# Optimization experiments

Hardware: AMD Instinct MI355X
Metric: run time of the kernel (lower is better)

## Reference

```python
import jax, jax.numpy as jnp
import numpy as np

K = 9                # snake kernel size
CENTER = K // 2
EXT = 1.0            # extend_scope
EPS = 1e-5           # GroupNorm eps (torch default)


def conv2d(x, w, b, stride, padding):
    out = jax.lax.conv_general_dilated(
        x, w, window_strides=stride, padding=padding,
        dimension_numbers=("NCHW", "OIHW", "NCHW"))
    return out + b[None, :, None, None]


def group_norm(x, gamma, beta, groups):
    B, C, H, W = x.shape
    xg = x.reshape(B, groups, C // groups, H, W)
    mu = xg.mean(axis=(2, 3, 4), keepdims=True)
    var = xg.var(axis=(2, 3, 4), keepdims=True)
    xn = ((xg - mu) / jnp.sqrt(var + EPS)).reshape(B, C, H, W)
    return xn * gamma[None, :, None, None] + beta[None, :, None, None]


def setup_inputs() -> dict:
    key = jax.random.key(0)
    ks = jax.random.split(key, 6)
    B, Cin, Cout, H, W = 4, 64, 64, 128, 128
    x = jax.random.normal(ks[0], (B, Cin, H, W), jnp.float32)
    w_off = jax.random.normal(ks[1], (2 * K, Cin, 3, 3), jnp.float32) * 0.05
    b_off = jax.random.normal(ks[2], (2 * K,), jnp.float32) * 0.01
    g_gn_off = jnp.ones((2 * K,), jnp.float32)
    b_gn_off = jnp.zeros((2 * K,), jnp.float32)
    w_dsc = jax.random.normal(ks[3], (Cout, Cin, K, 1), jnp.float32) * 0.05
    b_dsc = jax.random.normal(ks[4], (Cout,), jnp.float32) * 0.01
    g_gn = jnp.ones((Cout,), jnp.float32)
    b_gn = jnp.zeros((Cout,), jnp.float32)
    return {"x": x, "w_off": w_off, "b_off": b_off,
            "g_gn_off": g_gn_off, "b_gn_off": b_gn_off,
            "w_dsc": w_dsc, "b_dsc": b_dsc, "g_gn": g_gn, "b_gn": b_gn}


def reference(x, w_off, b_off, g_gn_off, b_gn_off, w_dsc, b_dsc, g_gn, b_gn):
    B, Cin, H, W = x.shape
    # offset branch: conv3x3 -> GN(K groups over 2K chans) -> tanh
    off = conv2d(x, w_off, b_off, (1, 1), "SAME")
    off = jnp.tanh(group_norm(off, g_gn_off, b_gn_off, K))
    y_off = off[:, :K]                              # morph=0 uses y offsets, [B,K,H,W]

    # cumulative offsets outward from the kernel center (center entry = 0)
    upper = jnp.cumsum(y_off[:, CENTER + 1:], axis=1)
    lower = jnp.flip(jnp.cumsum(jnp.flip(y_off[:, :CENTER], axis=1), axis=1), axis=1)
    y_off_new = jnp.concatenate(
        [lower, jnp.zeros_like(y_off[:, :1]), upper], axis=1)   # [B,K,H,W]

    # coordinate maps (pixel space)
    y_coord = jnp.arange(H, dtype=x.dtype)[None, None, :, None] + EXT * y_off_new
    x_spread = jnp.linspace(-CENTER, CENTER, K).astype(x.dtype)
    x_coord = jnp.broadcast_to(
        jnp.arange(W, dtype=x.dtype)[None, None, None, :]
        + x_spread[None, :, None, None], y_coord.shape)
    # rearrange b k h w -> b (h k) w
    y_map = y_coord.transpose(0, 2, 1, 3).reshape(B, H * K, W)
    x_map = x_coord.transpose(0, 2, 1, 3).reshape(B, H * K, W)

    # bilinear grid_sample, align_corners=True; clamp-to-range == torch's
    # _coordinate_map_scaling(clamp + [-1,1] normalize) then grid_sample
    yc = jnp.clip(y_map, 0.0, H - 1.0)
    xc = jnp.clip(x_map, 0.0, W - 1.0)
    y0 = jnp.floor(yc); x0 = jnp.floor(xc)
    wy = yc - y0; wx = xc - x0
    y0i = y0.astype(jnp.int32); x0i = x0.astype(jnp.int32)
    y1i = jnp.minimum(y0i + 1, H - 1); x1i = jnp.minimum(x0i + 1, W - 1)

    def samp(f, y0i, y1i, x0i, x1i, wy, wx):
        # f: [C,H,W]; indices/weights: [K*H, W] -> [C, K*H, W]
        v00 = f[:, y0i, x0i]; v01 = f[:, y0i, x1i]
        v10 = f[:, y1i, x0i]; v11 = f[:, y1i, x1i]
        return (v00 * (1 - wy) * (1 - wx) + v01 * (1 - wy) * wx
                + v10 * wy * (1 - wx) + v11 * wy * wx)

    deformed = jax.vmap(samp)(x, y0i, y1i, x0i, x1i, wy, wx)  # [B,C,K*H,W]

    # snake conv: kernel (K,1), stride (K,1), then GN(out//4) + ReLU
    out = conv2d(deformed, w_dsc, b_dsc, (K, 1), "VALID")      # [B,Cout,H,W]
    out = group_norm(out, g_gn, b_gn, w_dsc.shape[0] // 4)
    return jax.nn.relu(out)
```

## Files before the change

kernel.cpp:

```cpp
#include <hip/hip_runtime.h>
#include <hip/hip_bf16.h>
#include <math.h>

#define B 4
#define C 64
#define H 128
#define W 128
#define KK 9
#define CENTER 4
#define HW (H*W)
#define HP 130
#define WP 130

typedef __attribute__((ext_vector_type(8))) short short8;
typedef __attribute__((ext_vector_type(4))) float f4;

#define OFF_OFFT   0
#define OFF_XB     786432
#define OFF_WB     2949632
#define OFF_WOB    2968064
#define OFF_CSUM   2972672
#define OFF_OSUM   2980864

__device__ __forceinline__ unsigned bf16pack(float a, float b) {
    unsigned ua = __builtin_bit_cast(unsigned, a) + 0x8000u;
    unsigned ub = __builtin_bit_cast(unsigned, b) + 0x8000u;
    return __builtin_amdgcn_perm(ub, ua, 0x07060302);
}

__device__ __forceinline__ unsigned lerp_pack(unsigned a, unsigned b, float fw) {
    float alo = __builtin_bit_cast(float, a << 16);
    float ahi = __builtin_bit_cast(float, a & 0xffff0000u);
    float blo = __builtin_bit_cast(float, b << 16);
    float bhi = __builtin_bit_cast(float, b & 0xffff0000u);
    float slo = alo + fw * (blo - alo);
    float shi = ahi + fw * (bhi - ahi);
    return bf16pack(slo, shi);
}

__device__ __forceinline__ float fast_tanh(float x) {
    float e = __expf(2.f * x);
    return 1.f - 2.f * __builtin_amdgcn_rcpf(e + 1.f);
}

__global__ __launch_bounds__(256) void k_prep(const float* __restrict__ x,
                                              const float* __restrict__ w_dsc,
                                              const float* __restrict__ w_off,
                                              unsigned short* __restrict__ xb,
                                              unsigned short* __restrict__ wb,
                                              unsigned short* __restrict__ wob,
                                              float* __restrict__ csum) {
    int bid = blockIdx.x;
    int tid = threadIdx.x;
    if (bid < 2048) {
        __shared__ float lt[64 * 33];
        int xcd = bid & 7, i = bid >> 3;
        int c = i & 3, hc = (i >> 2) & 15, b = i >> 6;
        int h = (xcd << 4) | hc;
        int w0 = c * 32;
        int ciA = tid >> 2, gA = tid & 3;
        int wlB = tid >> 3, cgB = tid & 7;

        if (c == 0 && tid < 8)
            *(uint4*)(xb + ((size_t)(b * HP + h + 1) * WP) * 64 + tid * 8)
                = make_uint4(0, 0, 0, 0);
        if (c == 3 && tid < 8)
            *(uint4*)(xb + (((size_t)(b * HP + h + 1) * WP) + WP - 1) * 64 + tid * 8)
                = make_uint4(0, 0, 0, 0);
        {
            const float* src = x + ((size_t)(b * C + ciA) * HW) + h * W + w0 + gA * 8;
            float4 v0 = *(const float4*)src;
            float4 v1 = *(const float4*)(src + 4);
            float* d = lt + ciA * 33 + gA * 8;
            d[0] = v0.x; d[1] = v0.y; d[2] = v0.z; d[3] = v0.w;
            d[4] = v1.x; d[5] = v1.y; d[6] = v1.z; d[7] = v1.w;
        }
        __syncthreads();
        {
            unsigned u[4];
#pragma unroll
            for (int i2 = 0; i2 < 4; i2++) {
                float lo = lt[(cgB * 8 + 2 * i2)     * 33 + wlB];
                float hi = lt[(cgB * 8 + 2 * i2 + 1) * 33 + wlB];
                u[i2] = bf16pack(lo, hi);
            }
            *(uint4*)(xb + ((size_t)((b * HP + h + 1) * WP + w0 + wlB + 1)) * 64 + cgB * 8) =
                make_uint4(u[0], u[1], u[2], u[3]);
        }
    } else if (bid < 2048 + 8) {
        int r = bid - 2048;
        int b = r >> 1, which = r & 1;
        unsigned short* dst = xb + ((size_t)(b * HP + which * (HP - 1)) * WP) * 64;
        for (int t = tid; t < WP * 64 / 8; t += 256)
            *(uint4*)(dst + t * 8) = make_uint4(0, 0, 0, 0);
    } else if (bid < 2048 + 8 + 180) {
        int idx = (bid - (2048 + 8)) * 256 + tid;
        if (idx < KK * C * C) {
            int k  = idx >> 12;
            int r  = idx & 4095;
            int co = r >> 6;
            int ci = r & 63;
            unsigned u = __builtin_bit_cast(unsigned, w_dsc[(co * C + ci) * KK + k]);
            u = (u + 0x7fffu + ((u >> 16) & 1u)) >> 16;
            wb[idx] = (unsigned short)u;
        } else if (idx < KK * C * C + 9 * 16 * 64) {
            int r   = idx - KK * C * C;
            int tap = r >> 10;
            int j   = (r >> 6) & 15;
            int ci  = r & 63;
            float v = (j < 10) ? w_off[(j * C + ci) * 9 + tap] : 0.f;
            unsigned u = __builtin_bit_cast(unsigned, v);
            u = (u + 0x7fffu + ((u >> 16) & 1u)) >> 16;
            wob[r] = (unsigned short)u;
        }
    } else {
        int z = bid - (2048 + 8 + 180);
        int base = z * 1024 + tid * 4;
        *(f4*)(csum + base) = 0;
    }
}

__global__ __launch_bounds__(256, 4) void k_offconv(const unsigned short* __restrict__ xb,
                                                    const unsigned short* __restrict__ wob,
                                                    const float* __restrict__ b_off,
                                                    float* __restrict__ offT,
                                                    float* __restrict__ osum16) {
    __shared__ unsigned short wlds[1152 * 8];
    __shared__ float red[80];
    int bid = blockIdx.x;
    int xcd  = bid & 7;
    int i    = bid >> 3;
    int b    = i >> 5;
    int rest = i & 31;
    int h    = (xcd << 4) | (rest >> 1);
    int half = rest & 1;
    int tid  = threadIdx.x;
    int wid  = tid >> 6;
    int lane = tid & 63;
    int lm = lane & 15, qd = lane >> 4;
    int pw = half * 64 + wid * 16;

    for (int c = tid; c < 1152; c += 256) {
        int row = c >> 3, g = c & 7;
        uint4 v = *(const uint4*)(wob + c * 8);
        int dst = (g ^ (row & 7)) * 144 + row;
        *(uint4*)(wlds + dst * 8) = v;
    }
    __syncthreads();

    f4 acc = 0;
    const unsigned short* xrow = xb + ((size_t)(b * HP + h) * WP) * 64;
#pragma unroll
    for (int s = 0; s < 2; s++) {
        int co_ofs = s * 32 + qd * 8;
        short8 a_[9];
#pragma unroll
        for (int t = 0; t < 9; t++) {
            int ky = t / 3, kx = t - 3 * (t / 3);
            a_[t] = *(const short8*)(xrow +
                ((size_t)(ky * WP + pw + lm + kx)) * 64 + co_ofs);
        }
#pragma unroll
        for (int t = 0; t < 9; t++) {
            int row = t * 16 + lm;
            int chunk = (((s * 4 + qd) ^ (lm & 7)) * 144) + row;
            short8 w = *(const short8*)(wlds + chunk * 8);
            acc = __builtin_amdgcn_mfma_f32_16x16x32_bf16(a_[t], w, acc, 0, 0, 0);
        }
    }

    float bo = b_off[lm];
    float sv = 0.f, sq = 0.f;
    int pixbase = (b * H + h) * W;
#pragma unroll
    for (int r = 0; r < 4; r++) {
        float val = acc[r] + bo;
        int p = pw + qd * 4 + r;
        if (lm < 10) {
            offT[(size_t)(pixbase + p) * 12 + lm] = val;
            sv += val; sq += val * val;
        }
    }
    sv += __shfl_xor(sv, 16); sv += __shfl_xor(sv, 32);
    sq += __shfl_xor(sq, 16); sq += __shfl_xor(sq, 32);
    if (lane < 16 && lm < 10) {
        red[(wid * 10 + lm) * 2]     = sv;
        red[(wid * 10 + lm) * 2 + 1] = sq;
    }
    __syncthreads();
    if (tid < 20) {
        int j = tid >> 1, comp = tid & 1;
        float s = red[j * 2 + comp] + red[(10 + j) * 2 + comp] +
                  red[(20 + j) * 2 + comp] + red[(30 + j) * 2 + comp];
        int sidx = (h >> 3) & 15;
        atomicAdd(&osum16[sidx * 40 + b * 10 + (j >> 1) * 2 + comp], s);
    }
}

__global__ __launch_bounds__(256, 4) void k_main(const unsigned short* __restrict__ xb,
                                                 const float* __restrict__ offT,
                                                 const float* __restrict__ osum16,
                                                 const float* __restrict__ g_gn_off,
                                                 const float* __restrict__ b_gn_off,
                                                 const unsigned short* __restrict__ wb,
                                                 const float* __restrict__ b_dsc,
                                                 float* __restrict__ outp,
                                                 float* __restrict__ csum16) {
    __shared__ unsigned short wlds[2304 * 8];
    __shared__ float red[512];
    __shared__ float sred[16];

    int bid = blockIdx.x;
    int xcd  = bid & 7;
    int i    = bid >> 3;
    int b    = i >> 5;
    int rest = i & 31;
    int h    = (xcd << 4) | (rest >> 1);
    int p0   = (rest & 1) << 6;
    int tid  = threadIdx.x;
    int wid  = tid >> 6;
    int lane = tid & 63;
    int lm = lane & 15, qd = lane >> 4;

    int ps = p0 + wid * 16 + lm;

    if (tid < 160) {
        int gc = tid >> 4, s = tid & 15;
        float v = osum16[s * 40 + b * 10 + gc];
        v += __shfl_xor(v, 1); v += __shfl_xor(v, 2);
        v += __shfl_xor(v, 4); v += __shfl_xor(v, 8);
        if (s == 0) sred[gc] = v;
    }
    for (int c = tid; c < 2304; c += 256) {
        int k = c >> 8, row = (c >> 2) & 63, g2 = c & 3;
        uint4 v = *(const uint4*)(wb + (size_t)k * 4096 + row * 64 + g2 * 8);
        int dst = ((g2 ^ (row & 3)) * 576) + k * 64 + row;
        *(uint4*)(wlds + dst * 8) = v;
    }
    __syncthreads();

    float yoff[KK];
    {
        const float inv_n = 1.f / (2.f * HW);
        const float* op = offT + (size_t)((b * H + h) * W + ps) * 12;
        f4 o0 = *(const f4*)op;
        f4 o1 = *(const f4*)(op + 4);
        float o8 = op[8];
        float raw[KK] = {o0[0], o0[1], o0[2], o0[3], o1[0], o1[1], o1[2], o1[3], o8};
        float v[KK];
#pragma unroll
        for (int j = 0; j < KK; j++) {
            int g = j >> 1;
            float s  = sred[g * 2];
            float s2 = sred[g * 2 + 1];
            float mean = s * inv_n;
            float var  = s2 * inv_n - mean * mean;
            float rstd = rsqrtf(var + 1e-5f);
            v[j] = fast_tanh((raw[j] - mean) * rstd * g_gn_off[j] + b_gn_off[j]);
        }
        yoff[CENTER] = 0.f;
        float run = 0.f;
#pragma unroll
        for (int k = CENTER - 1; k >= 0; k--) { run += v[k]; yoff[k] = run; }
        run = 0.f;
#pragma unroll
        for (int k = CENTER + 1; k < KK; k++) { run += v[k]; yoff[k] = run; }
    }

    f4 acc[4];
#pragma unroll
    for (int ct = 0; ct < 4; ct++) acc[ct] = 0;

    auto kpass = [&](int s) {
        int so = s * 32;
#pragma unroll
        for (int kg = 0; kg < 3; kg++) {
            int   ofsA[3], ofsB[3];
            float fw[3];
#pragma unroll
            for (int j = 0; j < 3; j++) {
                int k = kg * 3 + j;
                float yc = fminf(fmaxf((float)h + yoff[k], 0.f), (float)(H - 1));
                float fy = floorf(yc);
                int y0 = (int)fy;
                int dy = (y0 < H - 1) ? (WP * 64) : 0;
                fw[j] = yc - fy;
                int xi = min(max(ps + k - CENTER, 0), W - 1);
                ofsA[j] = ((b * HP + y0 + 1) * WP + xi + 1) * 64 + qd * 8 + so;
                ofsB[j] = ofsA[j] + dy;
            }
            uint4 ga[3], gb[3];
#pragma unroll
            for (int j = 0; j < 3; j++) {
                ga[j] = *(const uint4*)(xb + ofsA[j]);
                gb[j] = *(const uint4*)(xb + ofsB[j]);
            }
#pragma unroll
            for (int j = 0; j < 3; j++) {
                int k = kg * 3 + j;
                uint4 r;
                r.x = lerp_pack(ga[j].x, gb[j].x, fw[j]);
                r.y = lerp_pack(ga[j].y, gb[j].y, fw[j]);
                r.z = lerp_pack(ga[j].z, gb[j].z, fw[j]);
                r.w = lerp_pack(ga[j].w, gb[j].w, fw[j]);
                short8 afr = __builtin_bit_cast(short8, r);
#pragma unroll
                for (int ct = 0; ct < 4; ct++) {
                    int row = ct * 16 + lm;
                    int chunk = ((qd ^ (lm & 3)) * 576) + k * 64 + row;
                    short8 bfr = *(const short8*)(wlds + chunk * 8);
                    acc[ct] = __builtin_amdgcn_mfma_f32_16x16x32_bf16(afr, bfr,
                                                                      acc[ct], 0, 0, 0);
                }
            }
        }
    };

    kpass(0);
    __syncthreads();
    for (int c = tid; c < 2304; c += 256) {
        int k = c >> 8, row = (c >> 2) & 63, g2 = c & 3;
        uint4 v = *(const uint4*)(wb + (size_t)k * 4096 + row * 64 + (4 + g2) * 8);
        int dst = ((g2 ^ (row & 3)) * 576) + k * 64 + row;
        *(uint4*)(wlds + dst * 8) = v;
    }
    __syncthreads();
    kpass(1);

#pragma unroll
    for (int ct = 0; ct < 4; ct++) {
        int co = ct * 16 + lm;
        float bias = b_dsc[co];
        f4 v;
        float sv = 0.f, sq = 0.f;
#pragma unroll
        for (int r = 0; r < 4; r++) {
            v[r] = acc[ct][r] + bias;
            sv += v[r]; sq += v[r] * v[r];
        }
        *(f4*)(outp + ((size_t)(b * C + co)) * HW + h * W + p0 + wid * 16 + qd * 4) = v;
        sv += __shfl_xor(sv, 16); sv += __shfl_xor(sv, 32);
        sq += __shfl_xor(sq, 16); sq += __shfl_xor(sq, 32);
        if (lane < 16) {
            red[((wid * 4 + ct) * 16 + lm) * 2]     = sv;
            red[((wid * 4 + ct) * 16 + lm) * 2 + 1] = sq;
        }
    }
    __syncthreads();
    if (tid < 128) {
        int co = tid >> 1, comp = tid & 1;
        int ct = co >> 4, lmr = co & 15;
        float s = 0.f;
#pragma unroll
        for (int w2 = 0; w2 < 4; w2++)
            s += red[((w2 * 4 + ct) * 16 + lmr) * 2 + comp];
        int sidx = (h >> 3) & 15;
        atomicAdd(&csum16[(sidx * 256 + b * 64 + co) * 2 + comp], s);
    }
}

__global__ __launch_bounds__(256) void k_norm(float* __restrict__ outp,
                                              const float* __restrict__ csum16,
                                              const float* __restrict__ g_gn,
                                              const float* __restrict__ b_gn) {
    __shared__ float lds[128];
    int bid = blockIdx.x;
    int xcd = bid & 7;
    int i   = bid >> 3;
    int bc  = i >> 1;
    int c2  = (xcd << 1) | (i & 1);
    int b = bc >> 6, co = bc & 63;
    int grp = co >> 2;
    int tid = threadIdx.x;

    if (tid < 128) {
        int s = tid >> 3, c = (tid >> 1) & 3, comp = tid & 1;
        lds[tid] = csum16[(s * 256 + b * 64 + grp * 4 + c) * 2 + comp];
    }
    __syncthreads();
#pragma unroll
    for (int st = 64; st >= 2; st >>= 1) {
        if (tid < st) lds[tid] += lds[tid + st];
        __syncthreads();
    }
    float S = lds[0], S2 = lds[1];
    float n = 4.f * HW;
    float mean = S / n;
    float var  = S2 / n - mean * mean;
    float rstd = rsqrtf(var + 1e-5f);
    float sc = rstd * g_gn[co];
    float sh = b_gn[co] - mean * sc;

    int idx = (bc * 16 + c2) * 256 + tid;
    float4* ptr = (float4*)outp;
    float4 vv = ptr[idx];
    vv.x = fmaxf(vv.x * sc + sh, 0.f);
    vv.y = fmaxf(vv.y * sc + sh, 0.f);
    vv.z = fmaxf(vv.z * sc + sh, 0.f);
    vv.w = fmaxf(vv.w * sc + sh, 0.f);
    ptr[idx] = vv;
}

extern "C" void kernel_launch(void* const* d_in, const int* in_sizes, int n_in,
                              void* d_out, int out_size, void* d_ws, size_t ws_size,
                              hipStream_t stream) {
    const float* x        = (const float*)d_in[0];
    const float* w_off    = (const float*)d_in[1];
    const float* b_off    = (const float*)d_in[2];
    const float* g_gn_off = (const float*)d_in[3];
    const float* b_gn_off = (const float*)d_in[4];
    const float* w_dsc    = (const float*)d_in[5];
    const float* b_dsc    = (const float*)d_in[6];
    const float* g_gn     = (const float*)d_in[7];
    const float* b_gn     = (const float*)d_in[8];
    float* out = (float*)d_out;
    float* ws  = (float*)d_ws;

    float*          offT   = ws + OFF_OFFT;
    unsigned short* xbp    = (unsigned short*)(ws + OFF_XB);
    unsigned short* wbp    = (unsigned short*)(ws + OFF_WB);
    unsigned short* wobp   = (unsigned short*)(ws + OFF_WOB);
    float*          csum16 = ws + OFF_CSUM;
    float*          osum16 = ws + OFF_OSUM;

    k_prep<<<2048 + 8 + 180 + 9, 256, 0, stream>>>(x, w_dsc, w_off, xbp, wbp,
                                                   wobp, csum16);
    k_offconv<<<2 * B * H, 256, 0, stream>>>(xbp, wobp, b_off, offT, osum16);
    k_main<<<2 * B * H, 256, 0, stream>>>(xbp, offT, osum16, g_gn_off, b_gn_off,
                                          wbp, b_dsc, out, csum16);
    k_norm<<<B * C * HW / 4 / 256, 256, 0, stream>>>(out, csum16, g_gn, b_gn);
}
```

Baseline: 135.5 us.

## Fuse offset conv, snake conv and GroupNorm into one kernel with grid barriers

Merges k_offconv, k_main and k_norm into a single kernel that runs as one resident wave of 1024 blocks and uses two atomic-counter grid barriers for the two GroupNorm reductions. Offset-conv results stay in LDS instead of going through a global offT buffer. The snake-conv accumulators stay in registers until the final normalized ReLU store, which removes the separate read-modify-write pass over the 16 MB output and two kernel launches. The cost is spin-wait barrier overhead and a dependence on every block being co-resident; the spin has a timeout break that would give wrong results if residency fails.

```diff
diff --git a/kernel.cpp b/kernel.cpp
--- a/kernel.cpp
+++ b/kernel.cpp
@@ -21,6 +21,7 @@
 #define OFF_WOB    2968064
 #define OFF_CSUM   2972672
 #define OFF_OSUM   2980864
+#define OFF_BAR    (OFF_CSUM + 8960)
 
 __device__ __forceinline__ unsigned bf16pack(float a, float b) {
     unsigned ua = __builtin_bit_cast(unsigned, a) + 0x8000u;
@@ -41,6 +42,20 @@
 __device__ __forceinline__ float fast_tanh(float x) {
     float e = __expf(2.f * x);
     return 1.f - 2.f * __builtin_amdgcn_rcpf(e + 1.f);
+}
+
+__device__ __forceinline__ void grid_barrier(unsigned* bar, unsigned nblk) {
+    __syncthreads();
+    if (threadIdx.x == 0) {
+        __hip_atomic_fetch_add(bar, 1u, __ATOMIC_ACQ_REL, __HIP_MEMORY_SCOPE_AGENT);
+        unsigned spins = 0;
+        while (__hip_atomic_load(bar, __ATOMIC_ACQUIRE, __HIP_MEMORY_SCOPE_AGENT)
+               < nblk) {
+            if (++spins > 100000000u) break;
+        }
+    }
+    __syncthreads();
+    __threadfence();
 }
 
 __global__ __launch_bounds__(256) void k_prep(const float* __restrict__ x,
@@ -120,95 +135,26 @@
     }
 }
 
-__global__ __launch_bounds__(256, 4) void k_offconv(const unsigned short* __restrict__ xb,
-                                                    const unsigned short* __restrict__ wob,
-                                                    const float* __restrict__ b_off,
-                                                    float* __restrict__ offT,
-                                                    float* __restrict__ osum16) {
-    __shared__ unsigned short wlds[1152 * 8];
-    __shared__ float red[80];
-    int bid = blockIdx.x;
-    int xcd  = bid & 7;
-    int i    = bid >> 3;
-    int b    = i >> 5;
-    int rest = i & 31;
-    int h    = (xcd << 4) | (rest >> 1);
-    int half = rest & 1;
-    int tid  = threadIdx.x;
-    int wid  = tid >> 6;
-    int lane = tid & 63;
-    int lm = lane & 15, qd = lane >> 4;
-    int pw = half * 64 + wid * 16;
-
-    for (int c = tid; c < 1152; c += 256) {
-        int row = c >> 3, g = c & 7;
-        uint4 v = *(const uint4*)(wob + c * 8);
-        int dst = (g ^ (row & 7)) * 144 + row;
-        *(uint4*)(wlds + dst * 8) = v;
-    }
-    __syncthreads();
-
-    f4 acc = 0;
-    const unsigned short* xrow = xb + ((size_t)(b * HP + h) * WP) * 64;
-#pragma unroll
-    for (int s = 0; s < 2; s++) {
-        int co_ofs = s * 32 + qd * 8;
-        short8 a_[9];
-#pragma unroll
-        for (int t = 0; t < 9; t++) {
-            int ky = t / 3, kx = t - 3 * (t / 3);
-            a_[t] = *(const short8*)(xrow +
-                ((size_t)(ky * WP + pw + lm + kx)) * 64 + co_ofs);
-        }
-#pragma unroll
-        for (int t = 0; t < 9; t++) {
-            int row = t * 16 + lm;
-            int chunk = (((s * 4 + qd) ^ (lm & 7)) * 144) + row;
-            short8 w = *(const short8*)(wlds + chunk * 8);
-            acc = __builtin_amdgcn_mfma_f32_16x16x32_bf16(a_[t], w, acc, 0, 0, 0);
-        }
-    }
-
-    float bo = b_off[lm];
-    float sv = 0.f, sq = 0.f;
-    int pixbase = (b * H + h) * W;
-#pragma unroll
-    for (int r = 0; r < 4; r++) {
-        float val = acc[r] + bo;
-        int p = pw + qd * 4 + r;
-        if (lm < 10) {
-            offT[(size_t)(pixbase + p) * 12 + lm] = val;
-            sv += val; sq += val * val;
-        }
-    }
-    sv += __shfl_xor(sv, 16); sv += __shfl_xor(sv, 32);
-    sq += __shfl_xor(sq, 16); sq += __shfl_xor(sq, 32);
-    if (lane < 16 && lm < 10) {
-        red[(wid * 10 + lm) * 2]     = sv;
-        red[(wid * 10 + lm) * 2 + 1] = sq;
-    }
-    __syncthreads();
-    if (tid < 20) {
-        int j = tid >> 1, comp = tid & 1;
-        float s = red[j * 2 + comp] + red[(10 + j) * 2 + comp] +
-                  red[(20 + j) * 2 + comp] + red[(30 + j) * 2 + comp];
-        int sidx = (h >> 3) & 15;
-        atomicAdd(&osum16[sidx * 40 + b * 10 + (j >> 1) * 2 + comp], s);
-    }
-}
-
-__global__ __launch_bounds__(256, 4) void k_main(const unsigned short* __restrict__ xb,
-                                                 const float* __restrict__ offT,
-                                                 const float* __restrict__ osum16,
-                                                 const float* __restrict__ g_gn_off,
-                                                 const float* __restrict__ b_gn_off,
-                                                 const unsigned short* __restrict__ wb,
-                                                 const float* __restrict__ b_dsc,
-                                                 float* __restrict__ outp,
-                                                 float* __restrict__ csum16) {
+__global__ __launch_bounds__(256, 4) void k_fused(
+        const unsigned short* __restrict__ xb,
+        const unsigned short* __restrict__ wob,
+        const float* __restrict__ b_off,
+        float* __restrict__ osum16,
+        const float* __restrict__ g_gn_off,
+        const float* __restrict__ b_gn_off,
+        const unsigned short* __restrict__ wb,
+        const float* __restrict__ b_dsc,
+        float* __restrict__ outp,
+        float* __restrict__ csum16,
+        const float* __restrict__ g_gn,
+        const float* __restrict__ b_gn,
+        unsigned* __restrict__ bars) {
     __shared__ unsigned short wlds[2304 * 8];
     __shared__ float red[512];
     __shared__ float sred[16];
+    __shared__ float scs[64];
+    __shared__ float shs[64];
+    float* offlds = (float*)(wlds + 9216);
 
     int bid = blockIdx.x;
     int xcd  = bid & 7;
@@ -221,8 +167,64 @@
     int wid  = tid >> 6;
     int lane = tid & 63;
     int lm = lane & 15, qd = lane >> 4;
-
-    int ps = p0 + wid * 16 + lm;
+    int pw = p0 + wid * 16;
+
+    for (int c = tid; c < 1152; c += 256) {
+        int row = c >> 3, g = c & 7;
+        uint4 v = *(const uint4*)(wob + c * 8);
+        int dst = (g ^ (row & 7)) * 144 + row;
+        *(uint4*)(wlds + dst * 8) = v;
+    }
+    __syncthreads();
+
+    f4 oacc = 0;
+    const unsigned short* xrow = xb + ((size_t)(b * HP + h) * WP) * 64;
+#pragma unroll
+    for (int s = 0; s < 2; s++) {
+        int co_ofs = s * 32 + qd * 8;
+        short8 a_[9];
+#pragma unroll
+        for (int t = 0; t < 9; t++) {
+            int ky = t / 3, kx = t - 3 * (t / 3);
+            a_[t] = *(const short8*)(xrow +
+                ((size_t)(ky * WP + pw + lm + kx)) * 64 + co_ofs);
+        }
+#pragma unroll
+        for (int t = 0; t < 9; t++) {
+            int row = t * 16 + lm;
+            int chunk = (((s * 4 + qd) ^ (lm & 7)) * 144) + row;
+            short8 w = *(const short8*)(wlds + chunk * 8);
+            oacc = __builtin_amdgcn_mfma_f32_16x16x32_bf16(a_[t], w, oacc, 0, 0, 0);
+        }
+    }
+
+    {
+        float bo = b_off[lm];
+        float sv = 0.f, sq = 0.f;
+#pragma unroll
+        for (int r = 0; r < 4; r++) {
+            float val = oacc[r] + bo;
+            if (lm < 10) {
+                offlds[(wid * 16 + qd * 4 + r) * 10 + lm] = val;
+                sv += val; sq += val * val;
+            }
+        }
+        sv += __shfl_xor(sv, 16); sv += __shfl_xor(sv, 32);
+        sq += __shfl_xor(sq, 16); sq += __shfl_xor(sq, 32);
+        if (lane < 16 && lm < 10) {
+            red[(wid * 10 + lm) * 2]     = sv;
+            red[(wid * 10 + lm) * 2 + 1] = sq;
+        }
+    }
+    __syncthreads();
+    if (tid < 20) {
+        int j = tid >> 1, comp = tid & 1;
+        float s = red[j * 2 + comp] + red[(10 + j) * 2 + comp] +
+                  red[(20 + j) * 2 + comp] + red[(30 + j) * 2 + comp];
+        int sidx = (h >> 3) & 15;
+        atomicAdd(&osum16[sidx * 40 + b * 10 + (j >> 1) * 2 + comp], s);
+    }
+    grid_barrier(bars + 0, 2 * B * H);
 
     if (tid < 160) {
         int gc = tid >> 4, s = tid & 15;
@@ -231,22 +233,25 @@
         v += __shfl_xor(v, 4); v += __shfl_xor(v, 8);
         if (s == 0) sred[gc] = v;
     }
+    int ps = p0 + wid * 16 + lm;
+    float raw[KK];
+    {
+        const float* op = offlds + (wid * 16 + lm) * 10;
+#pragma unroll
+        for (int j = 0; j < KK; j++) raw[j] = op[j];
+    }
+    __syncthreads();
+
     for (int c = tid; c < 2304; c += 256) {
         int k = c >> 8, row = (c >> 2) & 63, g2 = c & 3;
         uint4 v = *(const uint4*)(wb + (size_t)k * 4096 + row * 64 + g2 * 8);
         int dst = ((g2 ^ (row & 3)) * 576) + k * 64 + row;
         *(uint4*)(wlds + dst * 8) = v;
     }
-    __syncthreads();
 
     float yoff[KK];
     {
         const float inv_n = 1.f / (2.f * HW);
-        const float* op = offT + (size_t)((b * H + h) * W + ps) * 12;
-        f4 o0 = *(const f4*)op;
-        f4 o1 = *(const f4*)(op + 4);
-        float o8 = op[8];
-        float raw[KK] = {o0[0], o0[1], o0[2], o0[3], o1[0], o1[1], o1[2], o1[3], o8};
         float v[KK];
 #pragma unroll
         for (int j = 0; j < KK; j++) {
@@ -266,6 +271,7 @@
 #pragma unroll
         for (int k = CENTER + 1; k < KK; k++) { run += v[k]; yoff[k] = run; }
     }
+    __syncthreads();
 
     f4 acc[4];
 #pragma unroll
@@ -331,14 +337,12 @@
     for (int ct = 0; ct < 4; ct++) {
         int co = ct * 16 + lm;
         float bias = b_dsc[co];
-        f4 v;
         float sv = 0.f, sq = 0.f;
 #pragma unroll
         for (int r = 0; r < 4; r++) {
-            v[r] = acc[ct][r] + bias;
-            sv += v[r]; sq += v[r] * v[r];
-        }
-        *(f4*)(outp + ((size_t)(b * C + co)) * HW + h * W + p0 + wid * 16 + qd * 4) = v;
+            acc[ct][r] += bias;
+            sv += acc[ct][r]; sq += acc[ct][r] * acc[ct][r];
+        }
         sv += __shfl_xor(sv, 16); sv += __shfl_xor(sv, 32);
         sq += __shfl_xor(sq, 16); sq += __shfl_xor(sq, 32);
         if (lane < 16) {
@@ -357,48 +361,42 @@
         int sidx = (h >> 3) & 15;
         atomicAdd(&csum16[(sidx * 256 + b * 64 + co) * 2 + comp], s);
     }
-}
-
-__global__ __launch_bounds__(256) void k_norm(float* __restrict__ outp,
-                                              const float* __restrict__ csum16,
-                                              const float* __restrict__ g_gn,
-                                              const float* __restrict__ b_gn) {
-    __shared__ float lds[128];
-    int bid = blockIdx.x;
-    int xcd = bid & 7;
-    int i   = bid >> 3;
-    int bc  = i >> 1;
-    int c2  = (xcd << 1) | (i & 1);
-    int b = bc >> 6, co = bc & 63;
-    int grp = co >> 2;
-    int tid = threadIdx.x;
+    grid_barrier(bars + 1, 2 * B * H);
 
     if (tid < 128) {
-        int s = tid >> 3, c = (tid >> 1) & 3, comp = tid & 1;
-        lds[tid] = csum16[(s * 256 + b * 64 + grp * 4 + c) * 2 + comp];
-    }
-    __syncthreads();
-#pragma unroll
-    for (int st = 64; st >= 2; st >>= 1) {
-        if (tid < st) lds[tid] += lds[tid + st];
-        __syncthreads();
-    }
-    float S = lds[0], S2 = lds[1];
-    float n = 4.f * HW;
-    float mean = S / n;
-    float var  = S2 / n - mean * mean;
-    float rstd = rsqrtf(var + 1e-5f);
-    float sc = rstd * g_gn[co];
-    float sh = b_gn[co] - mean * sc;
-
-    int idx = (bc * 16 + c2) * 256 + tid;
-    float4* ptr = (float4*)outp;
-    float4 vv = ptr[idx];
-    vv.x = fmaxf(vv.x * sc + sh, 0.f);
-    vv.y = fmaxf(vv.y * sc + sh, 0.f);
-    vv.z = fmaxf(vv.z * sc + sh, 0.f);
-    vv.w = fmaxf(vv.w * sc + sh, 0.f);
-    ptr[idx] = vv;
+        int co = tid >> 1, comp = tid & 1;
+        float s = 0.f;
+#pragma unroll
+        for (int sx = 0; sx < 16; sx++)
+            s += csum16[(sx * 256 + b * 64 + co) * 2 + comp];
+        red[co * 2 + comp] = s;
+    }
+    __syncthreads();
+    if (tid < 64) {
+        int co = tid, grp = co >> 2;
+        float S  = red[grp * 8 + 0] + red[grp * 8 + 2] +
+                   red[grp * 8 + 4] + red[grp * 8 + 6];
+        float S2 = red[grp * 8 + 1] + red[grp * 8 + 3] +
+                   red[grp * 8 + 5] + red[grp * 8 + 7];
+        float n = 4.f * HW;
+        float mean = S / n;
+        float var  = S2 / n - mean * mean;
+        float rstd = rsqrtf(var + 1e-5f);
+        float sc = rstd * g_gn[co];
+        scs[co] = sc;
+        shs[co] = b_gn[co] - mean * sc;
+    }
+    __syncthreads();
+#pragma unroll
+    for (int ct = 0; ct < 4; ct++) {
+        int co = ct * 16 + lm;
+        float sc = scs[co], sh = shs[co];
+        f4 v;
+#pragma unroll
+        for (int r = 0; r < 4; r++)
+            v[r] = fmaxf(acc[ct][r] * sc + sh, 0.f);
+        *(f4*)(outp + ((size_t)(b * C + co)) * HW + h * W + p0 + wid * 16 + qd * 4) = v;
+    }
 }
 
 extern "C" void kernel_launch(void* const* d_in, const int* in_sizes, int n_in,
@@ -416,17 +414,16 @@
     float* out = (float*)d_out;
     float* ws  = (float*)d_ws;
 
-    float*          offT   = ws + OFF_OFFT;
     unsigned short* xbp    = (unsigned short*)(ws + OFF_XB);
     unsigned short* wbp    = (unsigned short*)(ws + OFF_WB);
     unsigned short* wobp   = (unsigned short*)(ws + OFF_WOB);
     float*          csum16 = ws + OFF_CSUM;
     float*          osum16 = ws + OFF_OSUM;
+    unsigned*       bars   = (unsigned*)(ws + OFF_BAR);
 
     k_prep<<<2048 + 8 + 180 + 9, 256, 0, stream>>>(x, w_dsc, w_off, xbp, wbp,
                                                    wobp, csum16);
-    k_offconv<<<2 * B * H, 256, 0, stream>>>(xbp, wobp, b_off, offT, osum16);
-    k_main<<<2 * B * H, 256, 0, stream>>>(xbp, offT, osum16, g_gn_off, b_gn_off,
-                                          wbp, b_dsc, out, csum16);
-    k_norm<<<B * C * HW / 4 / 256, 256, 0, stream>>>(out, csum16, g_gn, b_gn);
-}
+    k_fused<<<2 * B * H, 256, 0, stream>>>(xbp, wobp, b_off, osum16,
+                                           g_gn_off, b_gn_off, wbp, b_dsc,
+                                           out, csum16, g_gn, b_gn, bars);
+}
```

Result: slower. 478.8 us (+253.4%).

## Software-pipeline gathers in main kernel, hoist loads, coarsen prep blocks

Applied to the files above, without the earlier changes.

The main kernel now computes all nine sample offsets and weights once, then double-buffers the bilinear gather loads so the next tap group's global loads are issued before the current group's MFMAs. The offset load is hoisted above the GroupNorm stats read. The offset conv issues all 18 activation loads up front instead of per half. The prep kernel has each block process a full row (four chunks in a loop) rather than one chunk, giving four times fewer blocks. These are meant to hide gather latency and cut launch overhead, at the cost of more registers and possible occupancy loss.

```diff
diff --git a/kernel.cpp b/kernel.cpp
--- a/kernel.cpp
+++ b/kernel.cpp
@@ -52,49 +52,53 @@
                                               float* __restrict__ csum) {
     int bid = blockIdx.x;
     int tid = threadIdx.x;
-    if (bid < 2048) {
+    if (bid < 512) {
         __shared__ float lt[64 * 33];
         int xcd = bid & 7, i = bid >> 3;
-        int c = i & 3, hc = (i >> 2) & 15, b = i >> 6;
+        int hc = i & 15, b = i >> 4;
         int h = (xcd << 4) | hc;
-        int w0 = c * 32;
         int ciA = tid >> 2, gA = tid & 3;
         int wlB = tid >> 3, cgB = tid & 7;
 
-        if (c == 0 && tid < 8)
+        if (tid < 8) {
             *(uint4*)(xb + ((size_t)(b * HP + h + 1) * WP) * 64 + tid * 8)
                 = make_uint4(0, 0, 0, 0);
-        if (c == 3 && tid < 8)
             *(uint4*)(xb + (((size_t)(b * HP + h + 1) * WP) + WP - 1) * 64 + tid * 8)
                 = make_uint4(0, 0, 0, 0);
-        {
-            const float* src = x + ((size_t)(b * C + ciA) * HW) + h * W + w0 + gA * 8;
-            float4 v0 = *(const float4*)src;
-            float4 v1 = *(const float4*)(src + 4);
-            float* d = lt + ciA * 33 + gA * 8;
-            d[0] = v0.x; d[1] = v0.y; d[2] = v0.z; d[3] = v0.w;
-            d[4] = v1.x; d[5] = v1.y; d[6] = v1.z; d[7] = v1.w;
-        }
-        __syncthreads();
-        {
-            unsigned u[4];
-#pragma unroll
-            for (int i2 = 0; i2 < 4; i2++) {
-                float lo = lt[(cgB * 8 + 2 * i2)     * 33 + wlB];
-                float hi = lt[(cgB * 8 + 2 * i2 + 1) * 33 + wlB];
-                u[i2] = bf16pack(lo, hi);
+        }
+        const float* srcb = x + ((size_t)(b * C + ciA) * HW) + h * W + gA * 8;
+#pragma unroll
+        for (int c = 0; c < 4; c++) {
+            int w0 = c * 32;
+            float4 v0 = *(const float4*)(srcb + w0);
+            float4 v1 = *(const float4*)(srcb + w0 + 4);
+            __syncthreads();
+            {
+                float* d = lt + ciA * 33 + gA * 8;
+                d[0] = v0.x; d[1] = v0.y; d[2] = v0.z; d[3] = v0.w;
+                d[4] = v1.x; d[5] = v1.y; d[6] = v1.z; d[7] = v1.w;
             }
-            *(uint4*)(xb + ((size_t)((b * HP + h + 1) * WP + w0 + wlB + 1)) * 64 + cgB * 8) =
-                make_uint4(u[0], u[1], u[2], u[3]);
-        }
-    } else if (bid < 2048 + 8) {
-        int r = bid - 2048;
+            __syncthreads();
+            {
+                unsigned u[4];
+#pragma unroll
+                for (int i2 = 0; i2 < 4; i2++) {
+                    float lo = lt[(cgB * 8 + 2 * i2)     * 33 + wlB];
+                    float hi = lt[(cgB * 8 + 2 * i2 + 1) * 33 + wlB];
+                    u[i2] = bf16pack(lo, hi);
+                }
+                *(uint4*)(xb + ((size_t)((b * HP + h + 1) * WP + w0 + wlB + 1)) * 64
+                          + cgB * 8) = make_uint4(u[0], u[1], u[2], u[3]);
+            }
+        }
+    } else if (bid < 512 + 8) {
+        int r = bid - 512;
         int b = r >> 1, which = r & 1;
         unsigned short* dst = xb + ((size_t)(b * HP + which * (HP - 1)) * WP) * 64;
         for (int t = tid; t < WP * 64 / 8; t += 256)
             *(uint4*)(dst + t * 8) = make_uint4(0, 0, 0, 0);
-    } else if (bid < 2048 + 8 + 180) {
-        int idx = (bid - (2048 + 8)) * 256 + tid;
+    } else if (bid < 512 + 8 + 180) {
+        int idx = (bid - (512 + 8)) * 256 + tid;
         if (idx < KK * C * C) {
             int k  = idx >> 12;
             int r  = idx & 4095;
@@ -114,7 +118,7 @@
             wob[r] = (unsigned short)u;
         }
     } else {
-        int z = bid - (2048 + 8 + 180);
+        int z = bid - (512 + 8 + 180);
         int base = z * 1024 + tid * 4;
         *(f4*)(csum + base) = 0;
     }
@@ -150,23 +154,32 @@
 
     f4 acc = 0;
     const unsigned short* xrow = xb + ((size_t)(b * HP + h) * WP) * 64;
-#pragma unroll
-    for (int s = 0; s < 2; s++) {
-        int co_ofs = s * 32 + qd * 8;
-        short8 a_[9];
-#pragma unroll
-        for (int t = 0; t < 9; t++) {
-            int ky = t / 3, kx = t - 3 * (t / 3);
-            a_[t] = *(const short8*)(xrow +
-                ((size_t)(ky * WP + pw + lm + kx)) * 64 + co_ofs);
-        }
-#pragma unroll
-        for (int t = 0; t < 9; t++) {
-            int row = t * 16 + lm;
-            int chunk = (((s * 4 + qd) ^ (lm & 7)) * 144) + row;
-            short8 w = *(const short8*)(wlds + chunk * 8);
-            acc = __builtin_amdgcn_mfma_f32_16x16x32_bf16(a_[t], w, acc, 0, 0, 0);
-        }
+    short8 a0_[9], a1_[9];
+#pragma unroll
+    for (int t = 0; t < 9; t++) {
+        int ky = t / 3, kx = t - 3 * (t / 3);
+        a0_[t] = *(const short8*)(xrow +
+            ((size_t)(ky * WP + pw + lm + kx)) * 64 + qd * 8);
+    }
+#pragma unroll
+    for (int t = 0; t < 9; t++) {
+        int ky = t / 3, kx = t - 3 * (t / 3);
+        a1_[t] = *(const short8*)(xrow +
+            ((size_t)(ky * WP + pw + lm + kx)) * 64 + 32 + qd * 8);
+    }
+#pragma unroll
+    for (int t = 0; t < 9; t++) {
+        int row = t * 16 + lm;
+        int chunk = ((qd ^ (lm & 7)) * 144) + row;
+        short8 w = *(const short8*)(wlds + chunk * 8);
+        acc = __builtin_amdgcn_mfma_f32_16x16x32_bf16(a0_[t], w, acc, 0, 0, 0);
+    }
+#pragma unroll
+    for (int t = 0; t < 9; t++) {
+        int row = t * 16 + lm;
+        int chunk = (((4 + qd) ^ (lm & 7)) * 144) + row;
+        short8 w = *(const short8*)(wlds + chunk * 8);
+        acc = __builtin_amdgcn_mfma_f32_16x16x32_bf16(a1_[t], w, acc, 0, 0, 0);
     }
 
     float bo = b_off[lm];
@@ -196,6 +209,30 @@
         atomicAdd(&osum16[sidx * 40 + b * 10 + (j >> 1) * 2 + comp], s);
     }
 }
+
+#define LOADG(GA, GB, K0) do { _Pragma("unroll")                              \
+    for (int j = 0; j < 3; j++) {                                             \
+        GA[j] = *(const uint4*)(xb + oA[(K0) + j] + so);                      \
+        GB[j] = *(const uint4*)(xb + oB[(K0) + j] + so);                      \
+    } } while (0)
+
+#define CONSUME(GA, GB, K0) do { _Pragma("unroll")                            \
+    for (int j = 0; j < 3; j++) {                                             \
+        int k = (K0) + j;                                                     \
+        uint4 r;                                                              \
+        r.x = lerp_pack(GA[j].x, GB[j].x, fw9[k]);                            \
+        r.y = lerp_pack(GA[j].y, GB[j].y, fw9[k]);                            \
+        r.z = lerp_pack(GA[j].z, GB[j].z, fw9[k]);                            \
+        r.w = lerp_pack(GA[j].w, GB[j].w, fw9[k]);                            \
+        short8 afr = __builtin_bit_cast(short8, r);                           \
+        _Pragma("unroll")                                                     \
+        for (int ct = 0; ct < 4; ct++) {                                      \
+            int row = ct * 16 + lm;                                           \
+            int chunk = ((qd ^ (lm & 3)) * 576) + k * 64 + row;               \
+            short8 bfr = *(const short8*)(wlds + chunk * 8);                  \
+            acc[ct] = __builtin_amdgcn_mfma_f32_16x16x32_bf16(afr, bfr,       \
+                                                              acc[ct], 0, 0, 0); \
+        } } } while (0)
 
 __global__ __launch_bounds__(256, 4) void k_main(const unsigned short* __restrict__ xb,
                                                  const float* __restrict__ offT,
@@ -224,6 +261,11 @@
 
     int ps = p0 + wid * 16 + lm;
 
+    const float* op = offT + (size_t)((b * H + h) * W + ps) * 12;
+    f4 o0 = *(const f4*)op;
+    f4 o1 = *(const f4*)(op + 4);
+    float o8 = op[8];
+
     if (tid < 160) {
         int gc = tid >> 4, s = tid & 15;
         float v = osum16[s * 40 + b * 10 + gc];
@@ -242,10 +284,6 @@
     float yoff[KK];
     {
         const float inv_n = 1.f / (2.f * HW);
-        const float* op = offT + (size_t)((b * H + h) * W + ps) * 12;
-        f4 o0 = *(const f4*)op;
-        f4 o1 = *(const f4*)(op + 4);
-        float o8 = op[8];
         float raw[KK] = {o0[0], o0[1], o0[2], o0[3], o1[0], o1[1], o1[2], o1[3], o8};
         float v[KK];
 #pragma unroll
@@ -267,56 +305,35 @@
         for (int k = CENTER + 1; k < KK; k++) { run += v[k]; yoff[k] = run; }
     }
 
+    int oA[9], oB[9];
+    float fw9[9];
+#pragma unroll
+    for (int k = 0; k < 9; k++) {
+        float yc = fminf(fmaxf((float)h + yoff[k], 0.f), (float)(H - 1));
+        float fy = floorf(yc);
+        int y0 = (int)fy;
+        int dy = (y0 < H - 1) ? (WP * 64) : 0;
+        fw9[k] = yc - fy;
+        int xi = min(max(ps + k - CENTER, 0), W - 1);
+        oA[k] = ((b * HP + y0 + 1) * WP + xi + 1) * 64 + qd * 8;
+        oB[k] = oA[k] + dy;
+    }
+
     f4 acc[4];
 #pragma unroll
     for (int ct = 0; ct < 4; ct++) acc[ct] = 0;
 
-    auto kpass = [&](int s) {
-        int so = s * 32;
-#pragma unroll
-        for (int kg = 0; kg < 3; kg++) {
-            int   ofsA[3], ofsB[3];
-            float fw[3];
-#pragma unroll
-            for (int j = 0; j < 3; j++) {
-                int k = kg * 3 + j;
-                float yc = fminf(fmaxf((float)h + yoff[k], 0.f), (float)(H - 1));
-                float fy = floorf(yc);
-                int y0 = (int)fy;
-                int dy = (y0 < H - 1) ? (WP * 64) : 0;
-                fw[j] = yc - fy;
-                int xi = min(max(ps + k - CENTER, 0), W - 1);
-                ofsA[j] = ((b * HP + y0 + 1) * WP + xi + 1) * 64 + qd * 8 + so;
-                ofsB[j] = ofsA[j] + dy;
-            }
-            uint4 ga[3], gb[3];
-#pragma unroll
-            for (int j = 0; j < 3; j++) {
-                ga[j] = *(const uint4*)(xb + ofsA[j]);
-                gb[j] = *(const uint4*)(xb + ofsB[j]);
-            }
-#pragma unroll
-            for (int j = 0; j < 3; j++) {
-                int k = kg * 3 + j;
-                uint4 r;
-                r.x = lerp_pack(ga[j].x, gb[j].x, fw[j]);
-                r.y = lerp_pack(ga[j].y, gb[j].y, fw[j]);
-                r.z = lerp_pack(ga[j].z, gb[j].z, fw[j]);
-                r.w = lerp_pack(ga[j].w, gb[j].w, fw[j]);
-                short8 afr = __builtin_bit_cast(short8, r);
-#pragma unroll
-                for (int ct = 0; ct < 4; ct++) {
-                    int row = ct * 16 + lm;
-                    int chunk = ((qd ^ (lm & 3)) * 576) + k * 64 + row;
-                    short8 bfr = *(const short8*)(wlds + chunk * 8);
-                    acc[ct] = __builtin_amdgcn_mfma_f32_16x16x32_bf16(afr, bfr,
-                                                                      acc[ct], 0, 0, 0);
-                }
-            }
-        }
-    };
-
-    kpass(0);
+    {
+        const int so = 0;
+        uint4 gaA[3], gbA[3], gaB[3], gbB[3];
+        LOADG(gaA, gbA, 0);
+        LOADG(gaB, gbB, 3);
+        CONSUME(gaA, gbA, 0);
+        LOADG(gaA, gbA, 6);
+        CONSUME(gaB, gbB, 3);
+        CONSUME(gaA, gbA, 6);
+    }
+
     __syncthreads();
     for (int c = tid; c < 2304; c += 256) {
         int k = c >> 8, row = (c >> 2) & 63, g2 = c & 3;
@@ -325,7 +342,17 @@
         *(uint4*)(wlds + dst * 8) = v;
     }
     __syncthreads();
-    kpass(1);
+
+    {
+        const int so = 32;
+        uint4 gaA[3], gbA[3], gaB[3], gbB[3];
+        LOADG(gaA, gbA, 0);
+        LOADG(gaB, gbB, 3);
+        CONSUME(gaA, gbA, 0);
+        LOADG(gaA, gbA, 6);
+        CONSUME(gaB, gbB, 3);
+        CONSUME(gaA, gbA, 6);
+    }
 
 #pragma unroll
     for (int ct = 0; ct < 4; ct++) {
@@ -423,8 +450,8 @@
     float*          csum16 = ws + OFF_CSUM;
     float*          osum16 = ws + OFF_OSUM;
 
-    k_prep<<<2048 + 8 + 180 + 9, 256, 0, stream>>>(x, w_dsc, w_off, xbp, wbp,
-                                                   wobp, csum16);
+    k_prep<<<512 + 8 + 180 + 9, 256, 0, stream>>>(x, w_dsc, w_off, xbp, wbp,
+                                                  wobp, csum16);
     k_offconv<<<2 * B * H, 256, 0, stream>>>(xbp, wobp, b_off, offT, osum16);
     k_main<<<2 * B * H, 256, 0, stream>>>(xbp, offT, osum16, g_gn_off, b_gn_off,
                                           wbp, b_dsc, out, csum16);
```

After: 135.2 us. Within noise of the previous version (-0.2%).
